# Optimization experiments

Hardware: AMD Instinct MI355X
Metric: run time of the kernel (lower is better)

The kernel has to match this reference:

```python
import jax, jax.numpy as jnp
import numpy as np

Nx, Ny, Nu, Np = 8, 8, 2, 4
DELTA = 0.01
P = dict(alphaA=3.5, alphaB=1.1, pho=5.0, Cp=3.0, Ar=1.0, Ab=1.0,
         kr=1.0, kb=1.0, delH1=10.0, E1byR=3000.0, k1star=2.0e4,
         Td=310.0, Qr=200.0, Qb=200.0, CAf=1.0, Tf=320.0)
YMEAN = jnp.array([0.7, 0.5, 0.5, 310.0, 0.7, 0.5, 0.5, 310.0], jnp.float32)
YSTD  = jnp.array([0.3, 0.2, 0.2, 5.0, 0.3, 0.2, 0.2, 5.0], jnp.float32)
UMEAN = jnp.array([1.0, 0.5], jnp.float32)
USTD  = jnp.array([0.1, 0.05], jnp.float32)


def _fg(x, u):
    """Grey-box CSTR+flash ODE RHS in scaled coordinates. x:(B,8), u:(B,2)."""
    x = x * YSTD + YMEAN
    u = u * USTD + UMEAN
    Hr, CAr, CBr, Tr = x[..., 0:1], x[..., 1:2], x[..., 2:3], x[..., 3:4]
    Hb, CAb, CBb, Tb = x[..., 4:5], x[..., 5:6], x[..., 6:7], x[..., 7:8]
    F, D = u[..., 0:1], u[..., 1:2]
    den = P['alphaA'] * CAb + P['alphaB'] * CBb
    CAd = P['alphaA'] * CAb / den
    CBd = P['alphaB'] * CBb / den
    Fr = P['kr'] * jnp.sqrt(Hr)
    Fb = P['kb'] * jnp.sqrt(Hb)
    k1 = P['k1star'] * jnp.exp(-P['E1byR'] / Tr)
    r1 = k1 * CAr
    dHr  = (F + D - Fr) / P['Ar']
    dCAr = (F * (P['CAf'] - CAr) + D * (CAd - CAr)) / (P['Ar'] * Hr) - r1
    dCBr = (-F * CBr + D * (CBd - CBr)) / (P['Ar'] * Hr) + r1
    dTr  = (F * (P['Tf'] - Tr) + D * (P['Td'] - Tr)) / (P['Ar'] * Hr) \
           - P['Qr'] / (P['pho'] * P['Ar'] * P['Cp'] * Hr) \
           + r1 * P['delH1'] / (P['pho'] * P['Cp'])
    dHb  = (Fr - Fb - D) / P['Ab']
    dCAb = (Fr * (CAr - CAb) + D * (CAb - CAd)) / (P['Ab'] * Hb)
    dCBb = (Fr * (CBr - CBb) + D * (CBb - CBd)) / (P['Ab'] * Hb)
    dTb  = Fr * (Tr - Tb) / (P['Ab'] * Hb) + P['Qb'] / (P['pho'] * P['Ab'] * P['Cp'] * Hb)
    xdot = jnp.concatenate([dHr, dCAr, dCBr, dTr, dHb, dCAb, dCBb, dTb], axis=-1)
    return xdot / YSTD


def _fnn(h, Ws, bs):
    for W, b in zip(Ws[:-1], bs[:-1]):
        h = jnp.tanh(h @ W + b)
    return h @ Ws[-1] + bs[-1]


def _interp(yseq):
    # (B,(Np+1)*Ny) -> midpoint interpolation -> (B, Np*Ny)
    B = yseq.shape[0]
    y = yseq.reshape(B, Np + 1, Ny)
    return (0.5 * (y[:, :-1] + y[:, 1:])).reshape(B, Np * Ny)


def _cell(Ws, bs, xGz, u):
    xG, z = xGz[:, :Nx], xGz[:, Nx:]
    ypseq, upseq = z[:, :Np * Ny], z[:, Np * Ny:]
    k1 = _fg(xG, u) + _fnn(jnp.concatenate([xG, z, u], -1), Ws, bs)
    zi = jnp.concatenate([_interp(jnp.concatenate([ypseq, xG], -1)), upseq], -1)
    x2 = xG + DELTA * (k1 / 2)
    k2 = _fg(x2, u) + _fnn(jnp.concatenate([x2, zi, u], -1), Ws, bs)
    x3 = xG + DELTA * (k2 / 2)
    k3 = _fg(x3, u) + _fnn(jnp.concatenate([x3, zi, u], -1), Ws, bs)
    ypseqShifted = jnp.concatenate([ypseq[:, Ny:], xG], -1)
    zs = jnp.concatenate([ypseqShifted, upseq], -1)
    x4 = xG + DELTA * k3
    k4 = _fg(x4, u) + _fnn(jnp.concatenate([x4, zs, u], -1), Ws, bs)
    y = xG
    xGplus = xG + (DELTA / 6.0) * (k1 + 2 * k2 + 2 * k3 + k4)
    zplus = jnp.concatenate([ypseqShifted, upseq[:, Nu:], u], -1)
    return jnp.concatenate([xGplus, zplus], -1), y


def setup_inputs() -> dict:
    key = jax.random.key(0)
    ks = jax.random.split(key, 8)
    B, T = 8192, 256
    useq = jax.random.uniform(ks[0], (B, T, Nu), dtype=jnp.float32)
    xGz0 = jax.random.uniform(ks[1], (B, Nx + Np * (Ny + Nu)), dtype=jnp.float32)
    W1 = jax.random.normal(ks[2], (50, 64), jnp.float32) * (1.0 / np.sqrt(50.0))
    b1 = jnp.zeros((64,), jnp.float32)
    W2 = jax.random.normal(ks[3], (64, 64), jnp.float32) * (1.0 / 8.0)
    b2 = jnp.zeros((64,), jnp.float32)
    W3 = jax.random.normal(ks[4], (64, 8), jnp.float32) * 1e-3  # near-zero final kernel
    b3 = jnp.zeros((8,), jnp.float32)
    return {"useq": useq, "xGz0": xGz0, "W1": W1, "b1": b1,
            "W2": W2, "b2": b2, "W3": W3, "b3": b3}


def reference(useq, xGz0, W1, b1, W2, b2, W3, b3):
    Ws, bs = (W1, W2, W3), (b1, b2, b3)
    def step(carry, u_t):
        return _cell(Ws, bs, carry, u_t)
    _, ys = jax.lax.scan(step, xGz0, jnp.swapaxes(useq, 0, 1))  # ys: (T,B,Ny)
    return jnp.swapaxes(ys, 0, 1)  # (B,T,Ny)
```

## Files before the change

### kernel.cpp

```cpp
#include <hip/hip_runtime.h>


typedef _Float16 h2_t __attribute__((ext_vector_type(2)));
typedef _Float16 h8_t __attribute__((ext_vector_type(8)));
typedef __fp16  pk2_t __attribute__((ext_vector_type(2)));
typedef float f4_t __attribute__((ext_vector_type(4)));
typedef float f8_t __attribute__((ext_vector_type(8)));
typedef int   i4_t __attribute__((ext_vector_type(4)));

union H2I { h2_t h; pk2_t p; int i; float _f; };

#define DEVI __device__ __forceinline__

DEVI float rcp_f(float x) { return __builtin_amdgcn_rcpf(x); }
#if __has_builtin(__builtin_amdgcn_exp2f)
DEVI float exp2_f(float x) { return __builtin_amdgcn_exp2f(x); }
#else
DEVI float exp2_f(float x) { return __expf(x * 0.69314718056f); }
#endif
DEVI int pkrtz_i(float a, float b) { H2I u; u.p = __builtin_amdgcn_cvt_pkrtz(a, b); return u.i; }
DEVI int h2i(h2_t h) { H2I u; u.h = h; return u.i; }
DEVI h2_t i2h(int i) { H2I u; u.i = i; return u.h; }

#if __has_builtin(__builtin_elementwise_fma)
DEVI f8_t fma8(f8_t a, f8_t b, f8_t c) { return __builtin_elementwise_fma(a, b, c); }
#else
DEVI f8_t fma8(f8_t a, f8_t b, f8_t c) {
    f8_t r;
#pragma unroll
    for (int i = 0; i < 8; ++i) r[i] = fmaf(a[i], b[i], c[i]);
    return r;
}
#endif
DEVI f8_t splat8(float v) { f8_t r = { v, v, v, v, v, v, v, v }; return r; }

DEVI f4_t mfma16(h8_t a, h8_t b, f4_t c) {
    return __builtin_amdgcn_mfma_f32_16x16x32_f16(a, b, c, 0, 0, 0);
}

DEVI int chan_of(int ct, int rho) {
    int qr = rho >> 2, rr = rho & 3;
    return (ct < 2) ? (8 * qr + 4 * ct + rr)
                    : (32 + 8 * qr + 4 * (ct - 2) + rr);
}

DEVI f8_t fg_eval(f8_t x, float F, float D) {
    const f8_t ystd  = { 0.3f, 0.2f, 0.2f, 5.0f, 0.3f, 0.2f, 0.2f, 5.0f };
    const f8_t ymean = { 0.7f, 0.5f, 0.5f, 310.0f, 0.7f, 0.5f, 0.5f, 310.0f };
    f8_t xs = fma8(x, ystd, ymean);

    float Hr  = xs[0], CAr = xs[1], CBr = xs[2], Tr = xs[3];
    float Hb  = xs[4], CAb = xs[5], CBb = xs[6], Tb = xs[7];

    float aA = 3.5f * CAb, aB = 1.1f * CBb;
    float rden = rcp_f(aA + aB);
    float CAd = aA * rden, CBd = aB * rden;
    float Fr = __builtin_amdgcn_sqrtf(Hr);
    float Fb = __builtin_amdgcn_sqrtf(Hb);
    float rTr = rcp_f(Tr);
    float k1v = 20000.0f * __expf(-3000.0f * rTr);
    float r1 = k1v * CAr;
    float rHr = rcp_f(Hr), rHb = rcp_f(Hb);

    f8_t d;
    d[0] = F + D - Fr;
    d[1] = (F * (1.0f - CAr) + D * (CAd - CAr)) * rHr - r1;
    d[2] = (D * (CBd - CBr) - F * CBr) * rHr + r1;
    d[3] = (F * (320.0f - Tr) + D * (310.0f - Tr)) * rHr
         - (40.0f / 3.0f) * rHr + (2.0f / 3.0f) * r1;
    d[4] = Fr - Fb - D;
    d[5] = (Fr * (CAr - CAb) + D * (CAb - CAd)) * rHb;
    d[6] = (Fr * (CBr - CBb) + D * (CBb - CBd)) * rHb;
    d[7] = Fr * (Tr - Tb) * rHb + (40.0f / 3.0f) * rHb;

    const f8_t sc = { 10.0f / 3.0f, 5.0f, 5.0f, 0.2f,
                      10.0f / 3.0f, 5.0f, 5.0f, 0.2f };
    return d * sc;
}

struct Weights {
    h8_t a1[4][2], a2[4][2], a3[2];
    f4_t b1f[4], b2f[4], b3f;
};

DEVI int sigpair(float a, float b) {
    float s0 = rcp_f(1.0f + exp2_f(a));
    float s1 = rcp_f(1.0f + exp2_f(b));
    return pkrtz_i(s0, s1);
}

DEVI h8_t sig4(f4_t a0, f4_t a1) {
    i4_t g;
    g[0] = sigpair(a0[0], a0[1]);
    g[1] = sigpair(a0[2], a0[3]);
    g[2] = sigpair(a1[0], a1[1]);
    g[3] = sigpair(a1[2], a1[3]);
    return __builtin_bit_cast(h8_t, g);
}

DEVI i4_t avg4(i4_t A, i4_t B) {
    const h2_t half2c = { (_Float16)0.5f, (_Float16)0.5f };
    i4_t r;
#pragma unroll
    for (int i = 0; i < 4; ++i)
        r[i] = h2i((i2h(A[i]) + i2h(B[i])) * half2c);
    return r;
}

DEVI i4_t sel_f0y(i4_t V0, i4_t V1, i4_t V2, int q) {
    i4_t r;
#pragma unroll
    for (int i = 0; i < 4; ++i) {
        int t = (q == 2) ? V1[i] : V2[i];
        r[i] = (q == 1) ? V0[i] : t;
    }
    return r;
}
DEVI i4_t sel_f1(i4_t V3, i4_t f1c, int q) {
    i4_t r;
#pragma unroll
    for (int i = 0; i < 4; ++i)
        r[i] = (q == 0) ? V3[i] : f1c[i];
    return r;
}

DEVI f8_t eval_stage(f8_t x, i4_t f0y, i4_t f1w,
                     float F, float D, const Weights& W, int q) {
    f8_t kfg = fg_eval(x, F, D);

    i4_t f0w;
#pragma unroll
    for (int i = 0; i < 4; ++i) {
        int pxi = pkrtz_i(x[2 * i], x[2 * i + 1]);
        f0w[i] = (q == 0) ? pxi : f0y[i];
    }
    h8_t f0 = __builtin_bit_cast(h8_t, f0w);
    h8_t f1 = __builtin_bit_cast(h8_t, f1w);

    f4_t a0 = mfma16(W.a1[0][0], f0, W.b1f[0]); a0 = mfma16(W.a1[0][1], f1, a0);
    f4_t a1 = mfma16(W.a1[1][0], f0, W.b1f[1]); a1 = mfma16(W.a1[1][1], f1, a1);
    f4_t a2 = mfma16(W.a1[2][0], f0, W.b1f[2]); a2 = mfma16(W.a1[2][1], f1, a2);
    f4_t a3 = mfma16(W.a1[3][0], f0, W.b1f[3]); a3 = mfma16(W.a1[3][1], f1, a3);
    h8_t g0 = sig4(a0, a1);
    h8_t g1 = sig4(a2, a3);

    a0 = mfma16(W.a2[0][0], g0, W.b2f[0]); a0 = mfma16(W.a2[0][1], g1, a0);
    a1 = mfma16(W.a2[1][0], g0, W.b2f[1]); a1 = mfma16(W.a2[1][1], g1, a1);
    a2 = mfma16(W.a2[2][0], g0, W.b2f[2]); a2 = mfma16(W.a2[2][1], g1, a2);
    a3 = mfma16(W.a2[3][0], g0, W.b2f[3]); a3 = mfma16(W.a2[3][1], g1, a3);
    g0 = sig4(a0, a1);
    g1 = sig4(a2, a3);

    f4_t acc3 = mfma16(W.a3[0], g0, W.b3f);
    acc3 = mfma16(W.a3[1], g1, acc3);

    f8_t nn;
#pragma unroll
    for (int r = 0; r < 4; ++r) {
        int e = __float_as_int(acc3[r]);
        int o = e;
        asm("v_permlane16_swap_b32 %0, %1" : "+v"(e), "+v"(o));
        nn[r]     = __int_as_float(e);
        nn[4 + r] = __int_as_float(o);
    }

    return kfg + nn;
}

__global__ __launch_bounds__(64, 1)
void cstr_mfma1_kernel(const float* __restrict__ useq, const float* __restrict__ xGz0,
                       const float* __restrict__ W1, const float* __restrict__ b1,
                       const float* __restrict__ W2, const float* __restrict__ b2,
                       const float* __restrict__ W3, const float* __restrict__ b3,
                       float* __restrict__ out)
{
    const int lane = threadIdx.x & 63;
    const int m16 = lane & 15, q = lane >> 4;
    const int b0 = blockIdx.x * 16;

    const float S1 = 2.0f * 1.4426950408889634f;

    Weights W;
#pragma unroll
    for (int ct = 0; ct < 4; ++ct) {
        const int n = chan_of(ct, m16);
#pragma unroll
        for (int kh = 0; kh < 2; ++kh) {
            i4_t w1f, w2f;
#pragma unroll
            for (int jj = 0; jj < 4; ++jj) {
                int k0 = 32 * kh + 8 * q + 2 * jj;
                int k1 = k0 + 1;
                float v1a = (k0 < 50) ? S1 * W1[k0 * 64 + n] : 0.0f;
                float v1b = (k1 < 50) ? S1 * W1[k1 * 64 + n] : 0.0f;
                float v2a = -2.0f * S1 * W2[k0 * 64 + n];
                float v2b = -2.0f * S1 * W2[k1 * 64 + n];
                w1f[jj] = pkrtz_i(v1a, v1b);
                w2f[jj] = pkrtz_i(v2a, v2b);
            }
            W.a1[ct][kh] = __builtin_bit_cast(h8_t, w1f);
            W.a2[ct][kh] = __builtin_bit_cast(h8_t, w2f);
        }
        f4_t bb1, bb2;
#pragma unroll
        for (int r = 0; r < 4; ++r) {
            int ch = chan_of(ct, 4 * q + r);
            bb1[r] = S1 * b1[ch];
            float cs = 0.0f;
            for (int j = 0; j < 64; ++j) cs += W2[j * 64 + ch];
            bb2[r] = S1 * (b2[ch] + cs);
        }
        W.b1f[ct] = bb1;
        W.b2f[ct] = bb2;
    }
#pragma unroll
    for (int kh = 0; kh < 2; ++kh) {
        i4_t w3f;
#pragma unroll
        for (int jj = 0; jj < 4; ++jj) {
            int k0 = 32 * kh + 8 * q + 2 * jj;
            float va = -2.0f * W3[k0 * 8 + (m16 & 7)];
            float vb = -2.0f * W3[(k0 + 1) * 8 + (m16 & 7)];
            w3f[jj] = pkrtz_i(va, vb);
        }
        W.a3[kh] = __builtin_bit_cast(h8_t, w3f);
    }
    {
        f4_t bb3;
#pragma unroll
        for (int r = 0; r < 4; ++r) {
            int c = (4 * q + r) & 7;
            float cs = 0.0f;
            for (int j = 0; j < 64; ++j) cs += W3[j * 8 + c];
            bb3[r] = b3[c] + cs;
        }
        W.b3f = bb3;
    }

    const float* xz = xGz0 + (size_t)(b0 + m16) * 48;
    f8_t xg;
#pragma unroll
    for (int c = 0; c < 8; ++c) xg[c] = xz[c];
    i4_t P0, P1, P2, P3, U;
#pragma unroll
    for (int i = 0; i < 4; ++i) {
        P0[i] = pkrtz_i(xz[ 8 + 2 * i], xz[ 9 + 2 * i]);
        P1[i] = pkrtz_i(xz[16 + 2 * i], xz[17 + 2 * i]);
        P2[i] = pkrtz_i(xz[24 + 2 * i], xz[25 + 2 * i]);
        P3[i] = pkrtz_i(xz[32 + 2 * i], xz[33 + 2 * i]);
        U[i]  = pkrtz_i(xz[40 + 2 * i], xz[41 + 2 * i]);
    }

    const float2* ur = (const float2*)(useq + (size_t)(b0 + m16) * 512);
    float2* ow = (float2*)(out + (size_t)(b0 + m16) * 2048) + q;

    float2 uu = ur[0];

    const f8_t c005  = splat8(0.005f);
    const f8_t c01   = splat8(0.01f);
    const f8_t c2    = splat8(2.0f);
    const f8_t cD6   = splat8(0.0016666667f);

#pragma unroll 1
    for (int t = 0; t < 256; ++t) {
        const float2 uun = ur[(t + 1) & 255];

        {
            float s0 = (q == 0) ? xg[0] : (q == 1) ? xg[2] : (q == 2) ? xg[4] : xg[6];
            float s1 = (q == 0) ? xg[1] : (q == 1) ? xg[3] : (q == 2) ? xg[5] : xg[7];
            float2 st = { s0, s1 };
            ow[t * 4] = st;
        }

        const float u0 = uu.x, u1 = uu.y;
        const float F = fmaf(u0, 0.1f, 1.0f);
        const float D = fmaf(u1, 0.05f, 0.5f);
        const int upair_i = pkrtz_i(u0, u1);

        i4_t XC;
#pragma unroll
        for (int i = 0; i < 4; ++i) XC[i] = pkrtz_i(xg[2 * i], xg[2 * i + 1]);

        i4_t B0 = avg4(P0, P1), B1 = avg4(P1, P2),
             B2 = avg4(P2, P3), B3 = avg4(P3, XC);

        i4_t f1c;
#pragma unroll
        for (int i = 0; i < 4; ++i) {
            int t0 = (i == 0) ? ((q == 2) ? upair_i : 0) : 0;
            f1c[i] = (q == 1) ? U[i] : t0;
        }

        i4_t f0yA = sel_f0y(P0, P1, P2, q), f1A = sel_f1(P3, f1c, q);
        i4_t f0yB = sel_f0y(B0, B1, B2, q), f1B = sel_f1(B3, f1c, q);
        i4_t f0yC = sel_f0y(P1, P2, P3, q), f1C = sel_f1(XC, f1c, q);

        f8_t kc, ks, xv;
        kc = eval_stage(xg, f0yA, f1A, F, D, W, q);
        ks = kc;
        xv = fma8(c005, kc, xg);
        kc = eval_stage(xv, f0yB, f1B, F, D, W, q);
        ks = fma8(c2, kc, ks);
        xv = fma8(c005, kc, xg);
        kc = eval_stage(xv, f0yB, f1B, F, D, W, q);
        ks = fma8(c2, kc, ks);
        xv = fma8(c01, kc, xg);
        kc = eval_stage(xv, f0yC, f1C, F, D, W, q);

        ks = ks + kc;
        xg = fma8(cD6, ks, xg);

        P0 = P1; P1 = P2; P2 = P3; P3 = XC;
        {
            i4_t Un;
            Un[0] = U[1]; Un[1] = U[2]; Un[2] = U[3]; Un[3] = upair_i;
            U = Un;
        }

        uu = uun;
    }
}

extern "C" void kernel_launch(void* const* d_in, const int* in_sizes, int n_in,
                              void* d_out, int out_size, void* d_ws, size_t ws_size,
                              hipStream_t stream) {
    const float* useq = (const float*)d_in[0];
    const float* xGz0 = (const float*)d_in[1];
    const float* W1   = (const float*)d_in[2];
    const float* b1   = (const float*)d_in[3];
    const float* W2   = (const float*)d_in[4];
    const float* b2   = (const float*)d_in[5];
    const float* W3   = (const float*)d_in[6];
    const float* b3   = (const float*)d_in[7];
    float* out = (float*)d_out;

    cstr_mfma1_kernel<<<dim3(512), dim3(64), 0, stream>>>(
        useq, xGz0, W1, b1, W2, b2, W3, b3, out);
}
```

Baseline: 801.8 us.

## Interleave two independent batch groups per wave to hide MFMA latency

Each wave now integrates 32 samples as two independent 16-sample groups. Their RK4 stages are evaluated together, with MFMA and activation instructions interleaved so one group's dependency chain fills the stalls of the other. The grid is halved to keep total work the same. This trades wave-level parallelism for instruction-level parallelism and raises register pressure.

Measured after the change: 1.454 ms. 81.3% more time.

```diff
diff --git a/kernel.cpp b/kernel.cpp
--- a/kernel.cpp
+++ b/kernel.cpp
@@ -124,36 +124,14 @@
     return r;
 }
 
-DEVI f8_t eval_stage(f8_t x, i4_t f0y, i4_t f1w,
-                     float F, float D, const Weights& W, int q) {
-    f8_t kfg = fg_eval(x, F, D);
-
-    i4_t f0w;
-#pragma unroll
-    for (int i = 0; i < 4; ++i) {
-        int pxi = pkrtz_i(x[2 * i], x[2 * i + 1]);
-        f0w[i] = (q == 0) ? pxi : f0y[i];
-    }
-    h8_t f0 = __builtin_bit_cast(h8_t, f0w);
-    h8_t f1 = __builtin_bit_cast(h8_t, f1w);
-
-    f4_t a0 = mfma16(W.a1[0][0], f0, W.b1f[0]); a0 = mfma16(W.a1[0][1], f1, a0);
-    f4_t a1 = mfma16(W.a1[1][0], f0, W.b1f[1]); a1 = mfma16(W.a1[1][1], f1, a1);
-    f4_t a2 = mfma16(W.a1[2][0], f0, W.b1f[2]); a2 = mfma16(W.a1[2][1], f1, a2);
-    f4_t a3 = mfma16(W.a1[3][0], f0, W.b1f[3]); a3 = mfma16(W.a1[3][1], f1, a3);
-    h8_t g0 = sig4(a0, a1);
-    h8_t g1 = sig4(a2, a3);
-
-    a0 = mfma16(W.a2[0][0], g0, W.b2f[0]); a0 = mfma16(W.a2[0][1], g1, a0);
-    a1 = mfma16(W.a2[1][0], g0, W.b2f[1]); a1 = mfma16(W.a2[1][1], g1, a1);
-    a2 = mfma16(W.a2[2][0], g0, W.b2f[2]); a2 = mfma16(W.a2[2][1], g1, a2);
-    a3 = mfma16(W.a2[3][0], g0, W.b2f[3]); a3 = mfma16(W.a2[3][1], g1, a3);
-    g0 = sig4(a0, a1);
-    g1 = sig4(a2, a3);
-
-    f4_t acc3 = mfma16(W.a3[0], g0, W.b3f);
-    acc3 = mfma16(W.a3[1], g1, acc3);
-
+DEVI i4_t pack_pairs(f8_t x) {
+    i4_t r;
+#pragma unroll
+    for (int i = 0; i < 4; ++i) r[i] = pkrtz_i(x[2 * i], x[2 * i + 1]);
+    return r;
+}
+
+DEVI f8_t gather_add(f4_t acc3, f8_t kfg) {
     f8_t nn;
 #pragma unroll
     for (int r = 0; r < 4; ++r) {
@@ -163,8 +141,79 @@
         nn[r]     = __int_as_float(e);
         nn[4 + r] = __int_as_float(o);
     }
-
     return kfg + nn;
+}
+
+struct F8x2 { f8_t x, y; };
+
+DEVI F8x2 eval_duo(f8_t xX, i4_t pxX, i4_t f0yX, i4_t f1wX, float FX, float DX,
+                   f8_t xY, i4_t pxY, i4_t f0yY, i4_t f1wY, float FY, float DY,
+                   const Weights& W, int q) {
+    f8_t kfgX = fg_eval(xX, FX, DX);
+    f8_t kfgY = fg_eval(xY, FY, DY);
+
+    i4_t fwX, fwY;
+#pragma unroll
+    for (int i = 0; i < 4; ++i) {
+        fwX[i] = (q == 0) ? pxX[i] : f0yX[i];
+        fwY[i] = (q == 0) ? pxY[i] : f0yY[i];
+    }
+    h8_t f0X = __builtin_bit_cast(h8_t, fwX);
+    h8_t f1X = __builtin_bit_cast(h8_t, f1wX);
+    h8_t f0Y = __builtin_bit_cast(h8_t, fwY);
+    h8_t f1Y = __builtin_bit_cast(h8_t, f1wY);
+
+    f4_t aX0 = mfma16(W.a1[0][0], f0X, W.b1f[0]);
+    f4_t aY0 = mfma16(W.a1[0][0], f0Y, W.b1f[0]);
+    f4_t aX1 = mfma16(W.a1[1][0], f0X, W.b1f[1]);
+    f4_t aY1 = mfma16(W.a1[1][0], f0Y, W.b1f[1]);
+    f4_t aX2 = mfma16(W.a1[2][0], f0X, W.b1f[2]);
+    f4_t aY2 = mfma16(W.a1[2][0], f0Y, W.b1f[2]);
+    f4_t aX3 = mfma16(W.a1[3][0], f0X, W.b1f[3]);
+    f4_t aY3 = mfma16(W.a1[3][0], f0Y, W.b1f[3]);
+    aX0 = mfma16(W.a1[0][1], f1X, aX0);
+    aY0 = mfma16(W.a1[0][1], f1Y, aY0);
+    aX1 = mfma16(W.a1[1][1], f1X, aX1);
+    aY1 = mfma16(W.a1[1][1], f1Y, aY1);
+    aX2 = mfma16(W.a1[2][1], f1X, aX2);
+    aY2 = mfma16(W.a1[2][1], f1Y, aY2);
+    aX3 = mfma16(W.a1[3][1], f1X, aX3);
+    aY3 = mfma16(W.a1[3][1], f1Y, aY3);
+
+    h8_t g0X = sig4(aX0, aX1);
+    h8_t g0Y = sig4(aY0, aY1);
+    f4_t cX0 = mfma16(W.a2[0][0], g0X, W.b2f[0]);
+    f4_t cY0 = mfma16(W.a2[0][0], g0Y, W.b2f[0]);
+    f4_t cX1 = mfma16(W.a2[1][0], g0X, W.b2f[1]);
+    f4_t cY1 = mfma16(W.a2[1][0], g0Y, W.b2f[1]);
+    f4_t cX2 = mfma16(W.a2[2][0], g0X, W.b2f[2]);
+    f4_t cY2 = mfma16(W.a2[2][0], g0Y, W.b2f[2]);
+    f4_t cX3 = mfma16(W.a2[3][0], g0X, W.b2f[3]);
+    f4_t cY3 = mfma16(W.a2[3][0], g0Y, W.b2f[3]);
+    h8_t g1X = sig4(aX2, aX3);
+    h8_t g1Y = sig4(aY2, aY3);
+    cX0 = mfma16(W.a2[0][1], g1X, cX0);
+    cY0 = mfma16(W.a2[0][1], g1Y, cY0);
+    cX1 = mfma16(W.a2[1][1], g1X, cX1);
+    cY1 = mfma16(W.a2[1][1], g1Y, cY1);
+    cX2 = mfma16(W.a2[2][1], g1X, cX2);
+    cY2 = mfma16(W.a2[2][1], g1Y, cY2);
+    cX3 = mfma16(W.a2[3][1], g1X, cX3);
+    cY3 = mfma16(W.a2[3][1], g1Y, cY3);
+
+    h8_t h0X = sig4(cX0, cX1);
+    h8_t h0Y = sig4(cY0, cY1);
+    f4_t eX = mfma16(W.a3[0], h0X, W.b3f);
+    f4_t eY = mfma16(W.a3[0], h0Y, W.b3f);
+    h8_t h1X = sig4(cX2, cX3);
+    h8_t h1Y = sig4(cY2, cY3);
+    eX = mfma16(W.a3[1], h1X, eX);
+    eY = mfma16(W.a3[1], h1Y, eY);
+
+    F8x2 r;
+    r.x = gather_add(eX, kfgX);
+    r.y = gather_add(eY, kfgY);
+    return r;
 }
 
 __global__ __launch_bounds__(64, 1)
@@ -176,7 +225,7 @@
 {
     const int lane = threadIdx.x & 63;
     const int m16 = lane & 15, q = lane >> 4;
-    const int b0 = blockIdx.x * 16;
+    const int b0 = blockIdx.x * 32;
 
     const float S1 = 2.0f * 1.4426950408889634f;
 
@@ -237,24 +286,32 @@
         W.b3f = bb3;
     }
 
-    const float* xz = xGz0 + (size_t)(b0 + m16) * 48;
-    f8_t xg;
-#pragma unroll
-    for (int c = 0; c < 8; ++c) xg[c] = xz[c];
-    i4_t P0, P1, P2, P3, U;
+    const float* xzX = xGz0 + (size_t)(b0 + m16) * 48;
+    const float* xzY = xGz0 + (size_t)(b0 + 16 + m16) * 48;
+    f8_t xgX, xgY;
+#pragma unroll
+    for (int c = 0; c < 8; ++c) { xgX[c] = xzX[c]; xgY[c] = xzY[c]; }
+    i4_t P0X, P1X, P2X, P3X, UX, P0Y, P1Y, P2Y, P3Y, UY;
 #pragma unroll
     for (int i = 0; i < 4; ++i) {
-        P0[i] = pkrtz_i(xz[ 8 + 2 * i], xz[ 9 + 2 * i]);
-        P1[i] = pkrtz_i(xz[16 + 2 * i], xz[17 + 2 * i]);
-        P2[i] = pkrtz_i(xz[24 + 2 * i], xz[25 + 2 * i]);
-        P3[i] = pkrtz_i(xz[32 + 2 * i], xz[33 + 2 * i]);
-        U[i]  = pkrtz_i(xz[40 + 2 * i], xz[41 + 2 * i]);
-    }
-
-    const float2* ur = (const float2*)(useq + (size_t)(b0 + m16) * 512);
-    float2* ow = (float2*)(out + (size_t)(b0 + m16) * 2048) + q;
-
-    float2 uu = ur[0];
+        P0X[i] = pkrtz_i(xzX[ 8 + 2 * i], xzX[ 9 + 2 * i]);
+        P1X[i] = pkrtz_i(xzX[16 + 2 * i], xzX[17 + 2 * i]);
+        P2X[i] = pkrtz_i(xzX[24 + 2 * i], xzX[25 + 2 * i]);
+        P3X[i] = pkrtz_i(xzX[32 + 2 * i], xzX[33 + 2 * i]);
+        UX[i]  = pkrtz_i(xzX[40 + 2 * i], xzX[41 + 2 * i]);
+        P0Y[i] = pkrtz_i(xzY[ 8 + 2 * i], xzY[ 9 + 2 * i]);
+        P1Y[i] = pkrtz_i(xzY[16 + 2 * i], xzY[17 + 2 * i]);
+        P2Y[i] = pkrtz_i(xzY[24 + 2 * i], xzY[25 + 2 * i]);
+        P3Y[i] = pkrtz_i(xzY[32 + 2 * i], xzY[33 + 2 * i]);
+        UY[i]  = pkrtz_i(xzY[40 + 2 * i], xzY[41 + 2 * i]);
+    }
+
+    const float2* urX = (const float2*)(useq + (size_t)(b0 + m16) * 512);
+    const float2* urY = (const float2*)(useq + (size_t)(b0 + 16 + m16) * 512);
+    float2* owX = (float2*)(out + (size_t)(b0 + m16) * 2048) + q;
+    float2* owY = (float2*)(out + (size_t)(b0 + 16 + m16) * 2048) + q;
+
+    float2 uuX = urX[0], uuY = urY[0];
 
     const f8_t c005  = splat8(0.005f);
     const f8_t c01   = splat8(0.01f);
@@ -263,61 +320,83 @@
 
 #pragma unroll 1
     for (int t = 0; t < 256; ++t) {
-        const float2 uun = ur[(t + 1) & 255];
+        const float2 uunX = urX[(t + 1) & 255];
+        const float2 uunY = urY[(t + 1) & 255];
 
         {
-            float s0 = (q == 0) ? xg[0] : (q == 1) ? xg[2] : (q == 2) ? xg[4] : xg[6];
-            float s1 = (q == 0) ? xg[1] : (q == 1) ? xg[3] : (q == 2) ? xg[5] : xg[7];
+            float s0 = (q == 0) ? xgX[0] : (q == 1) ? xgX[2] : (q == 2) ? xgX[4] : xgX[6];
+            float s1 = (q == 0) ? xgX[1] : (q == 1) ? xgX[3] : (q == 2) ? xgX[5] : xgX[7];
             float2 st = { s0, s1 };
-            ow[t * 4] = st;
-        }
-
-        const float u0 = uu.x, u1 = uu.y;
-        const float F = fmaf(u0, 0.1f, 1.0f);
-        const float D = fmaf(u1, 0.05f, 0.5f);
-        const int upair_i = pkrtz_i(u0, u1);
-
-        i4_t XC;
-#pragma unroll
-        for (int i = 0; i < 4; ++i) XC[i] = pkrtz_i(xg[2 * i], xg[2 * i + 1]);
-
-        i4_t B0 = avg4(P0, P1), B1 = avg4(P1, P2),
-             B2 = avg4(P2, P3), B3 = avg4(P3, XC);
-
-        i4_t f1c;
+            owX[t * 4] = st;
+            s0 = (q == 0) ? xgY[0] : (q == 1) ? xgY[2] : (q == 2) ? xgY[4] : xgY[6];
+            s1 = (q == 0) ? xgY[1] : (q == 1) ? xgY[3] : (q == 2) ? xgY[5] : xgY[7];
+            float2 st2 = { s0, s1 };
+            owY[t * 4] = st2;
+        }
+
+        const float FX = fmaf(uuX.x, 0.1f, 1.0f);
+        const float DX = fmaf(uuX.y, 0.05f, 0.5f);
+        const int upX = pkrtz_i(uuX.x, uuX.y);
+        const float FY = fmaf(uuY.x, 0.1f, 1.0f);
+        const float DY = fmaf(uuY.y, 0.05f, 0.5f);
+        const int upY = pkrtz_i(uuY.x, uuY.y);
+
+        i4_t XCX = pack_pairs(xgX);
+        i4_t XCY = pack_pairs(xgY);
+
+        i4_t B0X = avg4(P0X, P1X), B1X = avg4(P1X, P2X),
+             B2X = avg4(P2X, P3X), B3X = avg4(P3X, XCX);
+        i4_t B0Y = avg4(P0Y, P1Y), B1Y = avg4(P1Y, P2Y),
+             B2Y = avg4(P2Y, P3Y), B3Y = avg4(P3Y, XCY);
+
+        i4_t f1cX, f1cY;
 #pragma unroll
         for (int i = 0; i < 4; ++i) {
-            int t0 = (i == 0) ? ((q == 2) ? upair_i : 0) : 0;
-            f1c[i] = (q == 1) ? U[i] : t0;
-        }
-
-        i4_t f0yA = sel_f0y(P0, P1, P2, q), f1A = sel_f1(P3, f1c, q);
-        i4_t f0yB = sel_f0y(B0, B1, B2, q), f1B = sel_f1(B3, f1c, q);
-        i4_t f0yC = sel_f0y(P1, P2, P3, q), f1C = sel_f1(XC, f1c, q);
-
-        f8_t kc, ks, xv;
-        kc = eval_stage(xg, f0yA, f1A, F, D, W, q);
-        ks = kc;
-        xv = fma8(c005, kc, xg);
-        kc = eval_stage(xv, f0yB, f1B, F, D, W, q);
-        ks = fma8(c2, kc, ks);
-        xv = fma8(c005, kc, xg);
-        kc = eval_stage(xv, f0yB, f1B, F, D, W, q);
-        ks = fma8(c2, kc, ks);
-        xv = fma8(c01, kc, xg);
-        kc = eval_stage(xv, f0yC, f1C, F, D, W, q);
-
-        ks = ks + kc;
-        xg = fma8(cD6, ks, xg);
-
-        P0 = P1; P1 = P2; P2 = P3; P3 = XC;
+            int t0 = (i == 0) ? ((q == 2) ? upX : 0) : 0;
+            f1cX[i] = (q == 1) ? UX[i] : t0;
+            int t1 = (i == 0) ? ((q == 2) ? upY : 0) : 0;
+            f1cY[i] = (q == 1) ? UY[i] : t1;
+        }
+
+        i4_t f0yAX = sel_f0y(P0X, P1X, P2X, q), f1AX = sel_f1(P3X, f1cX, q);
+        i4_t f0yBX = sel_f0y(B0X, B1X, B2X, q), f1BX = sel_f1(B3X, f1cX, q);
+        i4_t f0yCX = sel_f0y(P1X, P2X, P3X, q), f1CX = sel_f1(XCX, f1cX, q);
+        i4_t f0yAY = sel_f0y(P0Y, P1Y, P2Y, q), f1AY = sel_f1(P3Y, f1cY, q);
+        i4_t f0yBY = sel_f0y(B0Y, B1Y, B2Y, q), f1BY = sel_f1(B3Y, f1cY, q);
+        i4_t f0yCY = sel_f0y(P1Y, P2Y, P3Y, q), f1CY = sel_f1(XCY, f1cY, q);
+
+        f8_t ksX, ksY, xvX, xvY;
+        F8x2 k = eval_duo(xgX, XCX, f0yAX, f1AX, FX, DX,
+                          xgY, XCY, f0yAY, f1AY, FY, DY, W, q);
+        ksX = k.x;                 ksY = k.y;
+        xvX = fma8(c005, k.x, xgX); xvY = fma8(c005, k.y, xgY);
+        k = eval_duo(xvX, pack_pairs(xvX), f0yBX, f1BX, FX, DX,
+                     xvY, pack_pairs(xvY), f0yBY, f1BY, FY, DY, W, q);
+        ksX = fma8(c2, k.x, ksX);  ksY = fma8(c2, k.y, ksY);
+        xvX = fma8(c005, k.x, xgX); xvY = fma8(c005, k.y, xgY);
+        k = eval_duo(xvX, pack_pairs(xvX), f0yBX, f1BX, FX, DX,
+                     xvY, pack_pairs(xvY), f0yBY, f1BY, FY, DY, W, q);
+        ksX = fma8(c2, k.x, ksX);  ksY = fma8(c2, k.y, ksY);
+        xvX = fma8(c01, k.x, xgX);  xvY = fma8(c01, k.y, xgY);
+        k = eval_duo(xvX, pack_pairs(xvX), f0yCX, f1CX, FX, DX,
+                     xvY, pack_pairs(xvY), f0yCY, f1CY, FY, DY, W, q);
+
+        ksX = ksX + k.x;            ksY = ksY + k.y;
+        xgX = fma8(cD6, ksX, xgX);  xgY = fma8(cD6, ksY, xgY);
+
+        P0X = P1X; P1X = P2X; P2X = P3X; P3X = XCX;
+        P0Y = P1Y; P1Y = P2Y; P2Y = P3Y; P3Y = XCY;
         {
             i4_t Un;
-            Un[0] = U[1]; Un[1] = U[2]; Un[2] = U[3]; Un[3] = upair_i;
-            U = Un;
-        }
-
-        uu = uun;
+            Un[0] = UX[1]; Un[1] = UX[2]; Un[2] = UX[3]; Un[3] = upX;
+            UX = Un;
+            i4_t Um;
+            Um[0] = UY[1]; Um[1] = UY[2]; Um[2] = UY[3]; Um[3] = upY;
+            UY = Um;
+        }
+
+        uuX = uunX;
+        uuY = uunY;
     }
 }
 
@@ -334,6 +413,6 @@
     const float* b3   = (const float*)d_in[7];
     float* out = (float*)d_out;
 
-    cstr_mfma1_kernel<<<dim3(512), dim3(64), 0, stream>>>(
+    cstr_mfma1_kernel<<<dim3(256), dim3(64), 0, stream>>>(
         useq, xGz0, W1, b1, W2, b2, W3, b3, out);
 }
```
